# Kernel tuning notes

Hardware: AMD Instinct MI355X
Metric: run time of the kernel (lower is better)

## Reference

```python
import jax, jax.numpy as jnp
import numpy as np

N_NODES = 50000
DEG = 16
N_EDGES = N_NODES * DEG
IN_FEATS = 256
NUM_HEADS = 4
OUT_FEATS = 64
NEG_SLOPE = 0.2


def setup_inputs() -> dict:
    key = jax.random.key(0)
    k1, k2, k3, k4, k5, k6 = jax.random.split(key, 6)
    row_ptr = jnp.arange(N_NODES + 1, dtype=jnp.int64 if jax.config.jax_enable_x64 else jnp.int32) * DEG
    col_ind = jax.random.randint(k1, (N_EDGES,), 0, N_NODES)
    # CSC mirrors (used only by the fused op's backward pass; math-inert here)
    col_ptr = jnp.arange(N_NODES + 1, dtype=row_ptr.dtype) * DEG
    row_ind = jax.random.randint(k2, (N_EDGES,), 0, N_NODES)
    feat = jax.random.normal(k3, (N_NODES, IN_FEATS), dtype=jnp.float32)
    # Glorot-style init for params
    g = float(np.sqrt(2.0))  # gain for relu
    std_W = g * np.sqrt(2.0 / (IN_FEATS + OUT_FEATS * NUM_HEADS))
    W = jax.random.normal(k4, (IN_FEATS, OUT_FEATS * NUM_HEADS), dtype=jnp.float32) * std_W
    std_a = g * np.sqrt(2.0 / (1 + NUM_HEADS * OUT_FEATS))
    attn_l = jax.random.normal(k5, (1, NUM_HEADS, OUT_FEATS), dtype=jnp.float32) * std_a
    attn_r = jax.random.normal(k6, (1, NUM_HEADS, OUT_FEATS), dtype=jnp.float32) * std_a
    return {"row_ptr": row_ptr, "col_ind": col_ind, "col_ptr": col_ptr,
            "row_ind": row_ind, "feat": feat, "W": W, "attn_l": attn_l, "attn_r": attn_r}


def reference(row_ptr, col_ind, col_ptr, row_ind, feat, W, attn_l, attn_r):
    N = feat.shape[0]
    E = col_ind.shape[0]
    # Dense projection: [N, H, F]
    h = jnp.matmul(feat, W).reshape(N, NUM_HEADS, OUT_FEATS)
    attn_row = jnp.sum(attn_l * h, axis=-1)  # [N, H] (dst scores)
    attn_col = jnp.sum(attn_r * h, axis=-1)  # [N, H] (src scores)
    # Recover destination node id per edge from CSR row_ptr
    dst = jnp.searchsorted(row_ptr, jnp.arange(E), side="right") - 1  # [E]
    src = col_ind  # [E]
    # Edge score: LeakyReLU(attn_row[dst] + attn_col[src])
    e = attn_row[dst] + attn_col[src]  # [E, H]
    e = jnp.where(e > 0, e, NEG_SLOPE * e)
    # Segment softmax over each destination's neighborhood
    e_max = jax.ops.segment_max(e, dst, num_segments=N)  # [N, H]
    ex = jnp.exp(e - e_max[dst])  # [E, H]
    denom = jax.ops.segment_sum(ex, dst, num_segments=N)  # [N, H]
    alpha = ex / denom[dst]  # [E, H]
    # Weighted scatter-add aggregation of source features
    out = jax.ops.segment_sum(h[src] * alpha[:, :, None], dst, num_segments=N)  # [N, H, F]
    return out
```

## Files before the change

kernel.cpp:

```cpp
#include <hip/hip_runtime.h>
#include <hip/hip_bf16.h>

#define DEG        16
#define IN_FEATS   256
#define NUM_HEADS  4
#define OUT_FEATS  64
#define HF         256
#define NEG_SLOPE  0.2f

#define BM 64
#define BK 64
#define APITCH 72
#define BPITCH 72
#define CPITCH 264

typedef __attribute__((ext_vector_type(8))) short  short8;
typedef __attribute__((ext_vector_type(4))) float  floatx4;

__device__ __forceinline__ unsigned short f2bf(float f) {
    union { float f; unsigned u; } v; v.f = f;
    unsigned r = v.u + 0x7fffu + ((v.u >> 16) & 1u);
    return (unsigned short)(r >> 16);
}
__device__ __forceinline__ float bf2f(unsigned short u) {
    union { unsigned u; float f; } v; v.u = ((unsigned)u) << 16;
    return v.f;
}

__global__ __launch_bounds__(256) void conv_wt(
    const float* __restrict__ W, unsigned short* __restrict__ Wt)
{
    int n = blockIdx.x;
    int k = threadIdx.x;
    Wt[n * 256 + k] = f2bf(W[k * 256 + n]);
}

__global__ __launch_bounds__(256, 3) void gat_gemm_mfma(
    const float* __restrict__ A,
    const unsigned short* __restrict__ Bt,
    const float* __restrict__ attn_l,
    const float* __restrict__ attn_r,
    unsigned short* __restrict__ Hb,
    float* __restrict__ arow,
    float* __restrict__ acol,
    int M)
{
    __shared__ __align__(16) unsigned short SMEM[BM * APITCH + 256 * BPITCH];
    unsigned short* As = SMEM;
    unsigned short* Bs = SMEM + BM * APITCH;
    unsigned short* Cs = SMEM;

    const int tid  = threadIdx.x;
    const int wave = tid >> 6;
    const int lane = tid & 63;
    const int l15  = lane & 15;
    const int quad = lane >> 4;
    const int rowBase = blockIdx.x * BM;

    floatx4 acc[4][4] = {};

    for (int kt = 0; kt < IN_FEATS; kt += BK) {
        #pragma unroll
        for (int i = 0; i < 4; ++i) {
            int f  = tid + 256 * i;
            int r  = f >> 4;
            int c4 = (f & 15) << 2;
            int gr = rowBase + r;
            float4 va = (gr < M) ? *(const float4*)&A[(size_t)gr * IN_FEATS + kt + c4]
                                 : make_float4(0.f, 0.f, 0.f, 0.f);
            ushort4 pb;
            pb.x = f2bf(va.x); pb.y = f2bf(va.y);
            pb.z = f2bf(va.z); pb.w = f2bf(va.w);
            *(ushort4*)&As[r * APITCH + c4] = pb;
        }
        #pragma unroll
        for (int i = 0; i < 8; ++i) {
            int f  = tid + 256 * i;
            int n  = f >> 3;
            int k8 = (f & 7) << 3;
            uint4 v = *(const uint4*)&Bt[n * 256 + kt + k8];
            *(uint4*)&Bs[n * BPITCH + k8] = v;
        }
        __syncthreads();

        #pragma unroll
        for (int k0 = 0; k0 < BK; k0 += 32) {
            short8 af[4], bfr[4];
            #pragma unroll
            for (int mi = 0; mi < 4; ++mi)
                af[mi] = *(const short8*)&As[(mi * 16 + l15) * APITCH + k0 + quad * 8];
            #pragma unroll
            for (int ni = 0; ni < 4; ++ni)
                bfr[ni] = *(const short8*)&Bs[(wave * 64 + ni * 16 + l15) * BPITCH + k0 + quad * 8];
            #pragma unroll
            for (int mi = 0; mi < 4; ++mi)
                #pragma unroll
                for (int ni = 0; ni < 4; ++ni)
                    acc[mi][ni] = __builtin_amdgcn_mfma_f32_16x16x32_bf16(
                        af[mi], bfr[ni], acc[mi][ni], 0, 0, 0);
        }
        __syncthreads();
    }

    float al[4], ar[4];
    #pragma unroll
    for (int ni = 0; ni < 4; ++ni) {
        al[ni] = attn_l[wave * 64 + ni * 16 + l15];
        ar[ni] = attn_r[wave * 64 + ni * 16 + l15];
    }
    #pragma unroll
    for (int mi = 0; mi < 4; ++mi) {
        #pragma unroll
        for (int reg = 0; reg < 4; ++reg) {
            float pl = 0.f, pr = 0.f;
            #pragma unroll
            for (int ni = 0; ni < 4; ++ni) {
                pl = fmaf(acc[mi][ni][reg], al[ni], pl);
                pr = fmaf(acc[mi][ni][reg], ar[ni], pr);
            }
            #pragma unroll
            for (int off = 8; off >= 1; off >>= 1) {
                pl += __shfl_xor(pl, off, 64);
                pr += __shfl_xor(pr, off, 64);
            }
            if (l15 == 0) {
                int gr = rowBase + mi * 16 + quad * 4 + reg;
                if (gr < M) {
                    arow[gr * NUM_HEADS + wave] = pl;
                    acol[gr * NUM_HEADS + wave] = pr;
                }
            }
        }
    }

    #pragma unroll
    for (int mi = 0; mi < 4; ++mi)
        #pragma unroll
        for (int ni = 0; ni < 4; ++ni)
            #pragma unroll
            for (int reg = 0; reg < 4; ++reg)
                Cs[(mi * 16 + quad * 4 + reg) * CPITCH + wave * 64 + ni * 16 + l15] =
                    f2bf(acc[mi][ni][reg]);
    __syncthreads();

    #pragma unroll
    for (int i = 0; i < 8; ++i) {
        int f  = tid + 256 * i;
        int r  = f >> 5;
        int c8 = (f & 31) << 3;
        int gr = rowBase + r;
        if (gr < M) {
            uint4 v = *(const uint4*)&Cs[r * CPITCH + c8];
            *(uint4*)&Hb[(size_t)gr * HF + c8] = v;
        }
    }
}

__global__ __launch_bounds__(256) void gat_aggregate2(
    const unsigned short* __restrict__ Hb,
    const float* __restrict__ arow,
    const float* __restrict__ acol,
    const int* __restrict__ col_ind,
    float* __restrict__ out,
    int N)
{
    __shared__ float red[4][256];

    const int n = blockIdx.x;
    const int tid  = threadIdx.x;
    const int wave = tid >> 6;
    const int lane = tid & 63;
    const int j16  = lane & 15;
    const int hd16 = lane >> 4;

    int   src_e = col_ind[n * DEG + j16];
    float e = arow[n * NUM_HEADS + hd16] + acol[src_e * NUM_HEADS + hd16];
    e = (e > 0.f) ? e : NEG_SLOPE * e;

    float m = e;
    #pragma unroll
    for (int off = 8; off >= 1; off >>= 1)
        m = fmaxf(m, __shfl_xor(m, off, 16));
    float ex = __expf(e - m);
    float s = ex;
    #pragma unroll
    for (int off = 8; off >= 1; off >>= 1)
        s += __shfl_xor(s, off, 16);
    float alpha = ex / s;

    const int myHeadBase = (lane >> 4) << 4;
    float acc0 = 0.f, acc1 = 0.f, acc2 = 0.f, acc3 = 0.f;

    #pragma unroll
    for (int jj = 0; jj < 4; ++jj) {
        int j = wave * 4 + jj;
        int sj = __shfl(src_e, j, 64);
        float a = __shfl(alpha, myHeadBase + j, 64);
        uint2 v = *(const uint2*)&Hb[(size_t)sj * HF + lane * 4];
        acc0 = fmaf(a, bf2f((unsigned short)(v.x & 0xffffu)), acc0);
        acc1 = fmaf(a, bf2f((unsigned short)(v.x >> 16)),     acc1);
        acc2 = fmaf(a, bf2f((unsigned short)(v.y & 0xffffu)), acc2);
        acc3 = fmaf(a, bf2f((unsigned short)(v.y >> 16)),     acc3);
    }

    red[wave][lane * 4 + 0] = acc0;
    red[wave][lane * 4 + 1] = acc1;
    red[wave][lane * 4 + 2] = acc2;
    red[wave][lane * 4 + 3] = acc3;
    __syncthreads();

    out[(size_t)n * HF + tid] =
        red[0][tid] + red[1][tid] + red[2][tid] + red[3][tid];
}

extern "C" void kernel_launch(void* const* d_in, const int* in_sizes, int n_in,
                              void* d_out, int out_size, void* d_ws, size_t ws_size,
                              hipStream_t stream) {
    const int*   col_ind = (const int*)  d_in[1];
    const float* feat    = (const float*)d_in[4];
    const float* W       = (const float*)d_in[5];
    const float* attn_l  = (const float*)d_in[6];
    const float* attn_r  = (const float*)d_in[7];
    float* out = (float*)d_out;

    const int N = in_sizes[0] - 1;

    unsigned short* Hb = (unsigned short*)d_ws;
    float* arow = (float*)(Hb + (size_t)N * HF);
    float* acol = arow + (size_t)N * NUM_HEADS;
    unsigned short* Wt = (unsigned short*)(acol + (size_t)N * NUM_HEADS);

    conv_wt<<<256, 256, 0, stream>>>(W, Wt);

    dim3 ggrid((N + BM - 1) / BM);
    gat_gemm_mfma<<<ggrid, 256, 0, stream>>>(feat, Wt, attn_l, attn_r,
                                             Hb, arow, acol, N);

    gat_aggregate2<<<N, 256, 0, stream>>>(Hb, arow, acol, col_ind, out, N);
}
```

Measured before the change: 215.8 us.

## Pre-convert features to bf16 and load full A tile via global_load_lds

Adds a prep kernel that converts feat to bf16 (stored temporarily in the output buffer) alongside the W transpose. The GEMM then loads the whole 64x256 A tile into LDS with direct global-to-LDS loads using an XOR swizzle, and streams B fragments straight from global memory into registers with double buffering. This drops the per-K-tile syncs and the B staging through LDS. In exchange it adds an extra pass over feat to write bf16 and reuses d_out as scratch.

```diff
diff --git a/kernel.cpp b/kernel.cpp
--- a/kernel.cpp
+++ b/kernel.cpp
@@ -8,14 +8,11 @@
 #define HF         256
 #define NEG_SLOPE  0.2f
 
-#define BM 64
-#define BK 64
-#define APITCH 72
-#define BPITCH 72
 #define CPITCH 264
 
 typedef __attribute__((ext_vector_type(8))) short  short8;
 typedef __attribute__((ext_vector_type(4))) float  floatx4;
+typedef unsigned short ushortT;
 
 __device__ __forceinline__ unsigned short f2bf(float f) {
     union { float f; unsigned u; } v; v.f = f;
@@ -26,80 +23,102 @@
     union { unsigned u; float f; } v; v.u = ((unsigned)u) << 16;
     return v.f;
 }
-
-__global__ __launch_bounds__(256) void conv_wt(
-    const float* __restrict__ W, unsigned short* __restrict__ Wt)
+__device__ __forceinline__ unsigned pk2(float lo, float hi) {
+    return (unsigned)f2bf(lo) | ((unsigned)f2bf(hi) << 16);
+}
+
+__device__ __forceinline__ void load16_g2l(const void* g, void* lds) {
+    __builtin_amdgcn_global_load_lds(
+        (const __attribute__((address_space(1))) unsigned int*)(unsigned long long)g,
+        (__attribute__((address_space(3))) unsigned int*)(unsigned int)(unsigned long long)lds,
+        16, 0, 0);
+}
+
+__global__ __launch_bounds__(256) void prep(
+    const float* __restrict__ feat, const float* __restrict__ W,
+    ushortT* __restrict__ featb, ushortT* __restrict__ Wt,
+    int nfb, long long totalElems)
 {
-    int n = blockIdx.x;
-    int k = threadIdx.x;
-    Wt[n * 256 + k] = f2bf(W[k * 256 + n]);
-}
-
-__global__ __launch_bounds__(256, 3) void gat_gemm_mfma(
-    const float* __restrict__ A,
-    const unsigned short* __restrict__ Bt,
+    int b = blockIdx.x;
+    if (b < nfb) {
+        long long base = (long long)b * 2048 + (long long)threadIdx.x * 8;
+        if (base + 8 <= totalElems) {
+            float4 v0 = *(const float4*)&feat[base];
+            float4 v1 = *(const float4*)&feat[base + 4];
+            uint4 o;
+            o.x = pk2(v0.x, v0.y); o.y = pk2(v0.z, v0.w);
+            o.z = pk2(v1.x, v1.y); o.w = pk2(v1.z, v1.w);
+            *(uint4*)&featb[base] = o;
+        }
+    } else {
+        int n = b - nfb;
+        int k = threadIdx.x;
+        Wt[n * 256 + k] = f2bf(W[k * 256 + n]);
+    }
+}
+
+__global__ __launch_bounds__(256, 3) void gat_gemm_mfma2(
+    const ushortT* __restrict__ featb,
+    const ushortT* __restrict__ Bt,
     const float* __restrict__ attn_l,
     const float* __restrict__ attn_r,
-    unsigned short* __restrict__ Hb,
+    ushortT* __restrict__ Hb,
     float* __restrict__ arow,
     float* __restrict__ acol,
     int M)
 {
-    __shared__ __align__(16) unsigned short SMEM[BM * APITCH + 256 * BPITCH];
-    unsigned short* As = SMEM;
-    unsigned short* Bs = SMEM + BM * APITCH;
-    unsigned short* Cs = SMEM;
+    __shared__ __align__(16) ushortT SMEM[64 * CPITCH];
+    ushortT* As = SMEM;
+    ushortT* Cs = SMEM;
 
     const int tid  = threadIdx.x;
     const int wave = tid >> 6;
     const int lane = tid & 63;
     const int l15  = lane & 15;
     const int quad = lane >> 4;
-    const int rowBase = blockIdx.x * BM;
+    const int rowBase = blockIdx.x * 64;
+
+    #pragma unroll
+    for (int t = 0; t < 8; ++t) {
+        int row  = wave * 16 + t * 2 + (lane >> 5);
+        int cst  = lane & 31;
+        int cg   = cst ^ (row & 7);
+        int grow = rowBase + row; if (grow > M - 1) grow = M - 1;
+        const ushortT* g = featb + (long long)grow * 256 + cg * 8;
+        load16_g2l(g, &As[(wave * 512 + t * 64) * 8]);
+    }
+
+    short8 bbuf[2][4];
+    #pragma unroll
+    for (int ni = 0; ni < 4; ++ni)
+        bbuf[0][ni] = *(const short8*)&Bt[(wave * 64 + ni * 16 + l15) * 256 + quad * 8];
+
+    __syncthreads();
 
     floatx4 acc[4][4] = {};
 
-    for (int kt = 0; kt < IN_FEATS; kt += BK) {
-        #pragma unroll
-        for (int i = 0; i < 4; ++i) {
-            int f  = tid + 256 * i;
-            int r  = f >> 4;
-            int c4 = (f & 15) << 2;
-            int gr = rowBase + r;
-            float4 va = (gr < M) ? *(const float4*)&A[(size_t)gr * IN_FEATS + kt + c4]
-                                 : make_float4(0.f, 0.f, 0.f, 0.f);
-            ushort4 pb;
-            pb.x = f2bf(va.x); pb.y = f2bf(va.y);
-            pb.z = f2bf(va.z); pb.w = f2bf(va.w);
-            *(ushort4*)&As[r * APITCH + c4] = pb;
-        }
-        #pragma unroll
-        for (int i = 0; i < 8; ++i) {
-            int f  = tid + 256 * i;
-            int n  = f >> 3;
-            int k8 = (f & 7) << 3;
-            uint4 v = *(const uint4*)&Bt[n * 256 + kt + k8];
-            *(uint4*)&Bs[n * BPITCH + k8] = v;
-        }
-        __syncthreads();
-
-        #pragma unroll
-        for (int k0 = 0; k0 < BK; k0 += 32) {
-            short8 af[4], bfr[4];
-            #pragma unroll
-            for (int mi = 0; mi < 4; ++mi)
-                af[mi] = *(const short8*)&As[(mi * 16 + l15) * APITCH + k0 + quad * 8];
+    #pragma unroll
+    for (int ks = 0; ks < 8; ++ks) {
+        if (ks < 7) {
             #pragma unroll
             for (int ni = 0; ni < 4; ++ni)
-                bfr[ni] = *(const short8*)&Bs[(wave * 64 + ni * 16 + l15) * BPITCH + k0 + quad * 8];
-            #pragma unroll
-            for (int mi = 0; mi < 4; ++mi)
-                #pragma unroll
-                for (int ni = 0; ni < 4; ++ni)
-                    acc[mi][ni] = __builtin_amdgcn_mfma_f32_16x16x32_bf16(
-                        af[mi], bfr[ni], acc[mi][ni], 0, 0, 0);
-        }
-        __syncthreads();
+                bbuf[(ks + 1) & 1][ni] = *(const short8*)
+                    &Bt[(wave * 64 + ni * 16 + l15) * 256 + (ks + 1) * 32 + quad * 8];
+        }
+        short8 af[4];
+        #pragma unroll
+        for (int mi = 0; mi < 4; ++mi) {
+            int row = mi * 16 + l15;
+            int q   = ks * 4 + quad;
+            int cst = q ^ (row & 7);
+            af[mi] = *(const short8*)&As[row * 256 + cst * 8];
+        }
+        #pragma unroll
+        for (int mi = 0; mi < 4; ++mi)
+            #pragma unroll
+            for (int ni = 0; ni < 4; ++ni)
+                acc[mi][ni] = __builtin_amdgcn_mfma_f32_16x16x32_bf16(
+                    af[mi], bbuf[ks & 1][ni], acc[mi][ni], 0, 0, 0);
     }
 
     float al[4], ar[4];
@@ -133,6 +152,8 @@
         }
     }
 
+    __syncthreads();
+
     #pragma unroll
     for (int mi = 0; mi < 4; ++mi)
         #pragma unroll
@@ -157,7 +178,7 @@
 }
 
 __global__ __launch_bounds__(256) void gat_aggregate2(
-    const unsigned short* __restrict__ Hb,
+    const ushortT* __restrict__ Hb,
     const float* __restrict__ arow,
     const float* __restrict__ acol,
     const int* __restrict__ col_ind,
@@ -225,16 +246,20 @@
 
     const int N = in_sizes[0] - 1;
 
-    unsigned short* Hb = (unsigned short*)d_ws;
-    float* arow = (float*)(Hb + (size_t)N * HF);
-    float* acol = arow + (size_t)N * NUM_HEADS;
-    unsigned short* Wt = (unsigned short*)(acol + (size_t)N * NUM_HEADS);
-
-    conv_wt<<<256, 256, 0, stream>>>(W, Wt);
-
-    dim3 ggrid((N + BM - 1) / BM);
-    gat_gemm_mfma<<<ggrid, 256, 0, stream>>>(feat, Wt, attn_l, attn_r,
-                                             Hb, arow, acol, N);
+    ushortT* featb = (ushortT*)d_out;
+    ushortT* Hb    = (ushortT*)d_ws;
+    float*   arow  = (float*)(Hb + (size_t)N * HF);
+    float*   acol  = arow + (size_t)N * NUM_HEADS;
+    ushortT* Wt    = (ushortT*)(acol + (size_t)N * NUM_HEADS);
+
+    const long long totalElems = (long long)N * HF;
+    const int nfb = (int)((totalElems + 2047) / 2048);
+
+    prep<<<nfb + 256, 256, 0, stream>>>(feat, W, featb, Wt, nfb, totalElems);
+
+    dim3 ggrid((N + 63) / 64);
+    gat_gemm_mfma2<<<ggrid, 256, 0, stream>>>(featb, Wt, attn_l, attn_r,
+                                              Hb, arow, acol, N);
 
     gat_aggregate2<<<N, 256, 0, stream>>>(Hb, arow, acol, col_ind, out, N);
 }
```

New measurement: 198.9 us. 1.08x faster.
